# Kernel tuning notes

Measured on AMD Instinct MI355X. Metric: run time of the kernel, lower is better.

The kernel has to match this reference:

```python
import jax, jax.numpy as jnp
import numpy as np


def setup_inputs() -> dict:
    key = jax.random.key(0)
    ks = jax.random.split(key, 6)
    B, N, d = 8, 2048, 64
    h = jax.random.normal(ks[0], (B, N, d), dtype=jnp.float32)
    adj = jax.random.randint(ks[1], (B, N, N), 0, 2, dtype=jnp.int32)
    h_root = jax.random.normal(ks[2], (B, N), dtype=jnp.float32)
    weight = jax.random.normal(ks[3], (d, d), dtype=jnp.float32) * (1.0 / np.sqrt(d))
    a1 = jax.random.normal(ks[4], (d, 1), dtype=jnp.float32) * (1.0 / np.sqrt(d))
    a2 = jax.random.normal(ks[5], (d, 1), dtype=jnp.float32) * (1.0 / np.sqrt(d))
    return {"h": h, "adj": adj, "h_root": h_root, "weight": weight, "a1": a1, "a2": a2}


def reference(h, adj, h_root, weight, a1, a2):
    h0 = h
    hw = jax.nn.relu(jnp.matmul(h, weight))          # (B,N,d)
    t1 = jnp.matmul(hw, a1)                          # (B,N,1)
    t2 = jnp.matmul(hw, a2)                          # (B,N,1)
    # e[b,i,j] = relu(t1[b,i] + t2[b,j])  (broadcast, same as repeat/view in torch)
    e = jax.nn.relu(t1 + jnp.swapaxes(t2, -1, -2))   # (B,N,N)
    # FAITHFUL to source bug: pos0 = -9e15 * zeros_like(adj) == 0, so
    # non-edges get logit 0 (not -inf) before softmax.
    e = jnp.where(adj > 0, e, jnp.zeros_like(e))
    attention = jax.nn.softmax(e, axis=-1)           # (B,N,N)
    embedding = jnp.matmul(attention, hw)            # (B,N,d)
    # assign = h_root[:,:,None] @ ones(B,1,d) -> h_root broadcast over d;
    # assign > 0  <=>  h_root > 0 since ones are positive.
    assign = h_root[:, :, None] * jnp.ones((1, 1, hw.shape[-1]), dtype=hw.dtype)
    embedding = jnp.where(assign > 0, embedding, h0)
    return embedding
```

## Files before the change

kernel.cpp:

```cpp
#include <hip/hip_runtime.h>
#include <hip/hip_bf16.h>

#define BATCH 8
#define NN    2048
#define DD    64
#define BN    (BATCH * NN)
#define MWORDS 68

typedef __attribute__((ext_vector_type(8))) short bf16x8;
typedef __attribute__((ext_vector_type(4))) float f32x4;

static __device__ __forceinline__ unsigned f2bf_pk(float lo, float hi) {
  unsigned ul = __float_as_uint(lo);
  unsigned uh = __float_as_uint(hi);
  ul = (ul + 0x7fffu + ((ul >> 16) & 1u)) >> 16;
  uh = (uh + 0x7fffu + ((uh >> 16) & 1u)) & 0xffff0000u;
  return ul | uh;
}

__global__ __launch_bounds__(256) void kpack(
    const int* __restrict__ adj, const float* __restrict__ h_root,
    unsigned* __restrict__ masks) {
  const int row  = blockIdx.x * 4 + (threadIdx.x >> 6);
  const int lane = threadIdx.x & 63;
  if (h_root[row] <= 0.f) return;
  const int* ap = adj + (size_t)row * NN + lane * 32;
  unsigned word = 0;
#pragma unroll
  for (int i = 0; i < 8; ++i) {
    int4 v = *reinterpret_cast<const int4*>(ap + i * 4);
    word |= (v.x > 0 ? 1u : 0u) << (i * 4 + 0);
    word |= (v.y > 0 ? 1u : 0u) << (i * 4 + 1);
    word |= (v.z > 0 ? 1u : 0u) << (i * 4 + 2);
    word |= (v.w > 0 ? 1u : 0u) << (i * 4 + 3);
  }
  masks[(size_t)row * 64 + lane] = word;
}

__global__ __launch_bounds__(256) void k1_hw_t1_t2(
    const float* __restrict__ h, const float* __restrict__ W,
    const float* __restrict__ a1, const float* __restrict__ a2,
    unsigned short* __restrict__ hwT, float* __restrict__ t1, float* __restrict__ t2) {
  __shared__ float ht[64 * 36];
  __shared__ float Ws[64 * 64];
  __shared__ unsigned short bt[64 * 40];

  const int t  = threadIdx.x;
  const int r0 = blockIdx.x * 32;

#pragma unroll
  for (int r = 0; r < 4; ++r) {
    int f = t + 256 * r;
    reinterpret_cast<float4*>(Ws)[f] = reinterpret_cast<const float4*>(W)[f];
  }
#pragma unroll
  for (int r = 0; r < 2; ++r) {
    int f = t + 256 * r;
    int i = f >> 4, j4 = f & 15;
    float4 v = reinterpret_cast<const float4*>(h + (size_t)(r0 + i) * DD)[j4];
    ht[(4 * j4 + 0) * 36 + i] = v.x;
    ht[(4 * j4 + 1) * 36 + i] = v.y;
    ht[(4 * j4 + 2) * 36 + i] = v.z;
    ht[(4 * j4 + 3) * 36 + i] = v.w;
  }
  __syncthreads();

  const int trow = t >> 4, kcol = t & 15;
  float4 acc0 = make_float4(0.f, 0.f, 0.f, 0.f);
  float4 acc1 = make_float4(0.f, 0.f, 0.f, 0.f);

#pragma unroll 8
  for (int j = 0; j < 64; ++j) {
    float2 hv = *reinterpret_cast<const float2*>(&ht[j * 36 + 2 * trow]);
    float4 wv = reinterpret_cast<const float4*>(Ws)[j * 16 + kcol];
    acc0.x = fmaf(hv.x, wv.x, acc0.x); acc0.y = fmaf(hv.x, wv.y, acc0.y);
    acc0.z = fmaf(hv.x, wv.z, acc0.z); acc0.w = fmaf(hv.x, wv.w, acc0.w);
    acc1.x = fmaf(hv.y, wv.x, acc1.x); acc1.y = fmaf(hv.y, wv.y, acc1.y);
    acc1.z = fmaf(hv.y, wv.z, acc1.z); acc1.w = fmaf(hv.y, wv.w, acc1.w);
  }

  acc0.x = fmaxf(acc0.x, 0.f); acc0.y = fmaxf(acc0.y, 0.f);
  acc0.z = fmaxf(acc0.z, 0.f); acc0.w = fmaxf(acc0.w, 0.f);
  acc1.x = fmaxf(acc1.x, 0.f); acc1.y = fmaxf(acc1.y, 0.f);
  acc1.z = fmaxf(acc1.z, 0.f); acc1.w = fmaxf(acc1.w, 0.f);

  float4 a1v = reinterpret_cast<const float4*>(a1)[kcol];
  float4 a2v = reinterpret_cast<const float4*>(a2)[kcol];
  float s1_0 = acc0.x * a1v.x + acc0.y * a1v.y + acc0.z * a1v.z + acc0.w * a1v.w;
  float s1_1 = acc1.x * a1v.x + acc1.y * a1v.y + acc1.z * a1v.z + acc1.w * a1v.w;
  float s2_0 = acc0.x * a2v.x + acc0.y * a2v.y + acc0.z * a2v.z + acc0.w * a2v.w;
  float s2_1 = acc1.x * a2v.x + acc1.y * a2v.y + acc1.z * a2v.z + acc1.w * a2v.w;
#pragma unroll
  for (int mm = 1; mm <= 8; mm <<= 1) {
    s1_0 += __shfl_xor(s1_0, mm, 64);
    s1_1 += __shfl_xor(s1_1, mm, 64);
    s2_0 += __shfl_xor(s2_0, mm, 64);
    s2_1 += __shfl_xor(s2_1, mm, 64);
  }
  {
    int row = r0 + 2 * trow;
    if (kcol == 0) {
      t1[row] = s1_0; t1[row + 1] = s1_1;
      t2[row] = s2_0; t2[row + 1] = s2_1;
    }
  }

  {
    const float* a0 = &acc0.x;
    const float* a1p = &acc1.x;
#pragma unroll
    for (int c = 0; c < 4; ++c) {
      int k = 4 * kcol + c;
      *reinterpret_cast<unsigned*>(&bt[k * 40 + 2 * trow]) = f2bf_pk(a0[c], a1p[c]);
    }
  }
  __syncthreads();
  {
    int k = t >> 2, jp = t & 3;
    int g = k >> 4, n = k & 15;
    int bb = r0 >> 11;
    int jb = r0 & (NN - 1);
    int ks = jb >> 5;
    size_t base = ((((size_t)bb * (NN / 32) + ks) * 4 + g) * 64 + (jp * 16 + n)) * 8;
    *reinterpret_cast<int4*>(hwT + base) = *reinterpret_cast<const int4*>(&bt[k * 40 + jp * 8]);
  }
}

__global__ __launch_bounds__(256, 4) void k2_attn(
    const unsigned short* __restrict__ hwT, const unsigned* __restrict__ masks,
    const float* __restrict__ t1, const float* __restrict__ t2,
    const float* __restrict__ h, const float* __restrict__ h_root,
    float* __restrict__ out) {
  __shared__ unsigned maskS[16 * MWORDS];
  __shared__ float t2s[NN];
  __shared__ float os[4][16][68];
  __shared__ float denos[4][16];

  const int t    = threadIdx.x;
  const int b    = blockIdx.x >> 7;
  const int i0   = (blockIdx.x & 127) * 16;
  const int w    = t >> 6;
  const int lane = t & 63;
  const int m    = lane & 15;
  const int quad = lane >> 4;
  const int rowbase = b * NN + i0;

#pragma unroll
  for (int r = 0; r < 2; ++r)
    reinterpret_cast<float4*>(t2s)[t + 256 * r] =
        reinterpret_cast<const float4*>(t2 + b * NN)[t + 256 * r];

  {
    int row = t >> 4, w4 = t & 15;
    int4 mv = *reinterpret_cast<const int4*>(
        masks + ((size_t)(rowbase + row)) * 64 + w4 * 4);
    *reinterpret_cast<int4*>(&maskS[row * MWORDS + w4 * 4]) = mv;
  }
  __syncthreads();

  const float t1v = t1[rowbase + m];
  const int ks0 = w * 16;

  f32x4 acc[4];
#pragma unroll
  for (int g = 0; g < 4; ++g) acc[g] = (f32x4){0.f, 0.f, 0.f, 0.f};
  float den = 0.f;

  unsigned mcur = maskS[m * MWORDS + ks0];

#pragma unroll 1
  for (int kk = 0; kk < 16; ++kk) {
    const int ks = ks0 + kk;
    unsigned mnext = 0;
    if (kk + 1 < 16) mnext = maskS[m * MWORDS + ks + 1];

    const unsigned short* bp =
        hwT + ((((size_t)b * (NN / 32) + ks) * 4) * 64 + lane) * 8;
    bf16x8 B0 = *reinterpret_cast<const bf16x8*>(bp);
    bf16x8 B1 = *reinterpret_cast<const bf16x8*>(bp + 512);
    bf16x8 B2 = *reinterpret_cast<const bf16x8*>(bp + 1024);
    bf16x8 B3 = *reinterpret_cast<const bf16x8*>(bp + 1536);

    const float* t2p = &t2s[ks * 32 + quad * 8];
    float4 e0 = *reinterpret_cast<const float4*>(t2p);
    float4 e1 = *reinterpret_cast<const float4*>(t2p + 4);

    const unsigned mm8 = mcur >> (quad * 8);
    float p0 = (mm8 & 1u)   ? __expf(fmaxf(t1v + e0.x, 0.f)) : 1.f;
    float p1 = (mm8 & 2u)   ? __expf(fmaxf(t1v + e0.y, 0.f)) : 1.f;
    float p2 = (mm8 & 4u)   ? __expf(fmaxf(t1v + e0.z, 0.f)) : 1.f;
    float p3 = (mm8 & 8u)   ? __expf(fmaxf(t1v + e0.w, 0.f)) : 1.f;
    float p4 = (mm8 & 16u)  ? __expf(fmaxf(t1v + e1.x, 0.f)) : 1.f;
    float p5 = (mm8 & 32u)  ? __expf(fmaxf(t1v + e1.y, 0.f)) : 1.f;
    float p6 = (mm8 & 64u)  ? __expf(fmaxf(t1v + e1.z, 0.f)) : 1.f;
    float p7 = (mm8 & 128u) ? __expf(fmaxf(t1v + e1.w, 0.f)) : 1.f;
    den += ((p0 + p1) + (p2 + p3)) + ((p4 + p5) + (p6 + p7));

    union { bf16x8 v; unsigned u[4]; } Af;
    Af.u[0] = f2bf_pk(p0, p1); Af.u[1] = f2bf_pk(p2, p3);
    Af.u[2] = f2bf_pk(p4, p5); Af.u[3] = f2bf_pk(p6, p7);

    acc[0] = __builtin_amdgcn_mfma_f32_16x16x32_bf16(Af.v, B0, acc[0], 0, 0, 0);
    acc[1] = __builtin_amdgcn_mfma_f32_16x16x32_bf16(Af.v, B1, acc[1], 0, 0, 0);
    acc[2] = __builtin_amdgcn_mfma_f32_16x16x32_bf16(Af.v, B2, acc[2], 0, 0, 0);
    acc[3] = __builtin_amdgcn_mfma_f32_16x16x32_bf16(Af.v, B3, acc[3], 0, 0, 0);

    mcur = mnext;
  }

  den += __shfl_xor(den, 16, 64);
  den += __shfl_xor(den, 32, 64);
  if (quad == 0) denos[w][m] = den;

#pragma unroll
  for (int g = 0; g < 4; ++g)
#pragma unroll
    for (int r = 0; r < 4; ++r)
      os[w][quad * 4 + r][g * 16 + m] = acc[g][r];
  __syncthreads();

  {
    const int i = t >> 4, k4 = t & 15;
    float4 a = make_float4(0.f, 0.f, 0.f, 0.f);
    float d = 0.f;
#pragma unroll
    for (int ww = 0; ww < 4; ++ww) {
      float4 p = *reinterpret_cast<const float4*>(&os[ww][i][k4 * 4]);
      a.x += p.x; a.y += p.y; a.z += p.z; a.w += p.w;
      d += denos[ww][i];
    }
    const size_t row = (size_t)rowbase + i;
    float4 res;
    if (h_root[row] > 0.f) {
      const float inv = 1.f / d;
      res.x = a.x * inv; res.y = a.y * inv; res.z = a.z * inv; res.w = a.w * inv;
    } else {
      res = reinterpret_cast<const float4*>(h + row * DD)[k4];
    }
    reinterpret_cast<float4*>(out + row * DD)[k4] = res;
  }
}

extern "C" void kernel_launch(void* const* d_in, const int* in_sizes, int n_in,
                              void* d_out, int out_size, void* d_ws, size_t ws_size,
                              hipStream_t stream) {
  const float* h      = (const float*)d_in[0];
  const int*   adj    = (const int*)d_in[1];
  const float* h_root = (const float*)d_in[2];
  const float* W      = (const float*)d_in[3];
  const float* a1     = (const float*)d_in[4];
  const float* a2     = (const float*)d_in[5];
  float* out = (float*)d_out;

  unsigned short* hwT = (unsigned short*)d_ws;
  float* t1 = (float*)(hwT + (size_t)BN * DD);
  float* t2 = t1 + BN;
  unsigned* masks = (unsigned*)(t2 + BN);

  kpack<<<BN / 4, 256, 0, stream>>>(adj, h_root, masks);
  k1_hw_t1_t2<<<BN / 32, 256, 0, stream>>>(h, W, a1, a2, hwT, t1, t2);
  k2_attn<<<BATCH * (NN / 16), 256, 0, stream>>>(hwT, masks, t1, t2, h, h_root, out);
}
```

Before: 214.9 us.

## Merge mask packing into hw kernel and split attention into P-gen and GEMM

Mask packing and the hw/t1/t2 projection now run as one launch, with extra blocks doing the adjacency bit-packing, which saves a launch and lets both jobs share the GPU. The attention kernel is split in two. The first kernel computes the exp weights and row denominators and stores P as bf16 MFMA fragments in a global buffer. The second streams P and hwT through MFMA and normalises the result. The aim is to separate exp-heavy work from matrix-core work, at the cost of writing and re-reading a full B×N×N bf16 matrix through global memory.

```diff
diff --git a/kernel.cpp b/kernel.cpp
--- a/kernel.cpp
+++ b/kernel.cpp
@@ -18,29 +18,30 @@
   return ul | uh;
 }
 
-__global__ __launch_bounds__(256) void kpack(
-    const int* __restrict__ adj, const float* __restrict__ h_root,
-    unsigned* __restrict__ masks) {
-  const int row  = blockIdx.x * 4 + (threadIdx.x >> 6);
-  const int lane = threadIdx.x & 63;
-  if (h_root[row] <= 0.f) return;
-  const int* ap = adj + (size_t)row * NN + lane * 32;
-  unsigned word = 0;
-#pragma unroll
-  for (int i = 0; i < 8; ++i) {
-    int4 v = *reinterpret_cast<const int4*>(ap + i * 4);
-    word |= (v.x > 0 ? 1u : 0u) << (i * 4 + 0);
-    word |= (v.y > 0 ? 1u : 0u) << (i * 4 + 1);
-    word |= (v.z > 0 ? 1u : 0u) << (i * 4 + 2);
-    word |= (v.w > 0 ? 1u : 0u) << (i * 4 + 3);
-  }
-  masks[(size_t)row * 64 + lane] = word;
-}
-
-__global__ __launch_bounds__(256) void k1_hw_t1_t2(
+__global__ __launch_bounds__(256) void kA(
     const float* __restrict__ h, const float* __restrict__ W,
     const float* __restrict__ a1, const float* __restrict__ a2,
-    unsigned short* __restrict__ hwT, float* __restrict__ t1, float* __restrict__ t2) {
+    const int* __restrict__ adj, const float* __restrict__ h_root,
+    unsigned short* __restrict__ hwT, float* __restrict__ t1,
+    float* __restrict__ t2, unsigned* __restrict__ masks) {
+  if (blockIdx.x >= 512) {
+    const int row  = (blockIdx.x - 512) * 4 + (threadIdx.x >> 6);
+    const int lane = threadIdx.x & 63;
+    if (h_root[row] <= 0.f) return;
+    const int* ap = adj + (size_t)row * NN + lane * 32;
+    unsigned word = 0;
+#pragma unroll
+    for (int i = 0; i < 8; ++i) {
+      int4 v = *reinterpret_cast<const int4*>(ap + i * 4);
+      word |= (v.x > 0 ? 1u : 0u) << (i * 4 + 0);
+      word |= (v.y > 0 ? 1u : 0u) << (i * 4 + 1);
+      word |= (v.z > 0 ? 1u : 0u) << (i * 4 + 2);
+      word |= (v.w > 0 ? 1u : 0u) << (i * 4 + 3);
+    }
+    masks[(size_t)row * 64 + lane] = word;
+    return;
+  }
+
   __shared__ float ht[64 * 36];
   __shared__ float Ws[64 * 64];
   __shared__ unsigned short bt[64 * 40];
@@ -126,19 +127,19 @@
   }
 }
 
-__global__ __launch_bounds__(256, 4) void k2_attn(
-    const unsigned short* __restrict__ hwT, const unsigned* __restrict__ masks,
-    const float* __restrict__ t1, const float* __restrict__ t2,
-    const float* __restrict__ h, const float* __restrict__ h_root,
-    float* __restrict__ out) {
+__global__ __launch_bounds__(256, 4) void k2a_pgen(
+    const unsigned* __restrict__ masks, const float* __restrict__ t1,
+    const float* __restrict__ t2,
+    unsigned short* __restrict__ pfrag, float* __restrict__ den) {
   __shared__ unsigned maskS[16 * MWORDS];
   __shared__ float t2s[NN];
-  __shared__ float os[4][16][68];
-  __shared__ float denos[4][16];
+  __shared__ float t1s[16];
+  __shared__ float denP[4][16];
 
   const int t    = threadIdx.x;
-  const int b    = blockIdx.x >> 7;
-  const int i0   = (blockIdx.x & 127) * 16;
+  const int bid  = blockIdx.x;
+  const int b    = bid >> 7;
+  const int i0   = (bid & 127) * 16;
   const int w    = t >> 6;
   const int lane = t & 63;
   const int m    = lane & 15;
@@ -149,43 +150,29 @@
   for (int r = 0; r < 2; ++r)
     reinterpret_cast<float4*>(t2s)[t + 256 * r] =
         reinterpret_cast<const float4*>(t2 + b * NN)[t + 256 * r];
-
   {
     int row = t >> 4, w4 = t & 15;
     int4 mv = *reinterpret_cast<const int4*>(
-        masks + ((size_t)(rowbase + row)) * 64 + w4 * 4);
+        masks + (size_t)(rowbase + row) * 64 + w4 * 4);
     *reinterpret_cast<int4*>(&maskS[row * MWORDS + w4 * 4]) = mv;
   }
-  __syncthreads();
-
-  const float t1v = t1[rowbase + m];
+  if (t < 16) t1s[t] = t1[rowbase + t];
+  __syncthreads();
+
+  const float t1v = t1s[m];
   const int ks0 = w * 16;
-
-  f32x4 acc[4];
-#pragma unroll
-  for (int g = 0; g < 4; ++g) acc[g] = (f32x4){0.f, 0.f, 0.f, 0.f};
-  float den = 0.f;
-
-  unsigned mcur = maskS[m * MWORDS + ks0];
+  float den_acc = 0.f;
+  unsigned short* pout = pfrag + (((size_t)bid * 64 + ks0) * 64 + lane) * 8;
 
 #pragma unroll 1
   for (int kk = 0; kk < 16; ++kk) {
     const int ks = ks0 + kk;
-    unsigned mnext = 0;
-    if (kk + 1 < 16) mnext = maskS[m * MWORDS + ks + 1];
-
-    const unsigned short* bp =
-        hwT + ((((size_t)b * (NN / 32) + ks) * 4) * 64 + lane) * 8;
-    bf16x8 B0 = *reinterpret_cast<const bf16x8*>(bp);
-    bf16x8 B1 = *reinterpret_cast<const bf16x8*>(bp + 512);
-    bf16x8 B2 = *reinterpret_cast<const bf16x8*>(bp + 1024);
-    bf16x8 B3 = *reinterpret_cast<const bf16x8*>(bp + 1536);
-
+    const unsigned mw  = maskS[m * MWORDS + ks];
+    const unsigned mm8 = mw >> (quad * 8);
     const float* t2p = &t2s[ks * 32 + quad * 8];
     float4 e0 = *reinterpret_cast<const float4*>(t2p);
     float4 e1 = *reinterpret_cast<const float4*>(t2p + 4);
 
-    const unsigned mm8 = mcur >> (quad * 8);
     float p0 = (mm8 & 1u)   ? __expf(fmaxf(t1v + e0.x, 0.f)) : 1.f;
     float p1 = (mm8 & 2u)   ? __expf(fmaxf(t1v + e0.y, 0.f)) : 1.f;
     float p2 = (mm8 & 4u)   ? __expf(fmaxf(t1v + e0.z, 0.f)) : 1.f;
@@ -194,23 +181,63 @@
     float p5 = (mm8 & 32u)  ? __expf(fmaxf(t1v + e1.y, 0.f)) : 1.f;
     float p6 = (mm8 & 64u)  ? __expf(fmaxf(t1v + e1.z, 0.f)) : 1.f;
     float p7 = (mm8 & 128u) ? __expf(fmaxf(t1v + e1.w, 0.f)) : 1.f;
-    den += ((p0 + p1) + (p2 + p3)) + ((p4 + p5) + (p6 + p7));
-
-    union { bf16x8 v; unsigned u[4]; } Af;
-    Af.u[0] = f2bf_pk(p0, p1); Af.u[1] = f2bf_pk(p2, p3);
-    Af.u[2] = f2bf_pk(p4, p5); Af.u[3] = f2bf_pk(p6, p7);
-
-    acc[0] = __builtin_amdgcn_mfma_f32_16x16x32_bf16(Af.v, B0, acc[0], 0, 0, 0);
-    acc[1] = __builtin_amdgcn_mfma_f32_16x16x32_bf16(Af.v, B1, acc[1], 0, 0, 0);
-    acc[2] = __builtin_amdgcn_mfma_f32_16x16x32_bf16(Af.v, B2, acc[2], 0, 0, 0);
-    acc[3] = __builtin_amdgcn_mfma_f32_16x16x32_bf16(Af.v, B3, acc[3], 0, 0, 0);
-
-    mcur = mnext;
-  }
-
-  den += __shfl_xor(den, 16, 64);
-  den += __shfl_xor(den, 32, 64);
-  if (quad == 0) denos[w][m] = den;
+    den_acc += ((p0 + p1) + (p2 + p3)) + ((p4 + p5) + (p6 + p7));
+
+    int4 Af;
+    Af.x = (int)f2bf_pk(p0, p1);
+    Af.y = (int)f2bf_pk(p2, p3);
+    Af.z = (int)f2bf_pk(p4, p5);
+    Af.w = (int)f2bf_pk(p6, p7);
+    *reinterpret_cast<int4*>(pout + (size_t)kk * 512) = Af;
+  }
+
+  den_acc += __shfl_xor(den_acc, 16, 64);
+  den_acc += __shfl_xor(den_acc, 32, 64);
+  if (quad == 0) denP[w][m] = den_acc;
+  __syncthreads();
+  if (t < 16)
+    den[rowbase + t] = (denP[0][t] + denP[1][t]) + (denP[2][t] + denP[3][t]);
+}
+
+__global__ __launch_bounds__(256, 4) void k2b_gemm(
+    const unsigned short* __restrict__ hwT, const unsigned short* __restrict__ pfrag,
+    const float* __restrict__ den, const float* __restrict__ h,
+    const float* __restrict__ h_root, float* __restrict__ out) {
+  __shared__ float os[4][16][68];
+
+  const int t    = threadIdx.x;
+  const int bid  = blockIdx.x;
+  const int b    = bid >> 7;
+  const int i0   = (bid & 127) * 16;
+  const int w    = t >> 6;
+  const int lane = t & 63;
+  const int m    = lane & 15;
+  const int quad = lane >> 4;
+  const int rowbase = b * NN + i0;
+
+  f32x4 acc[4];
+#pragma unroll
+  for (int g = 0; g < 4; ++g) acc[g] = (f32x4){0.f, 0.f, 0.f, 0.f};
+
+  const int ks0 = w * 16;
+  const unsigned short* pin = pfrag + (((size_t)bid * 64 + ks0) * 64 + lane) * 8;
+  const unsigned short* bbase =
+      hwT + ((((size_t)b * (NN / 32) + ks0) * 4) * 64 + lane) * 8;
+
+#pragma unroll 1
+  for (int kk = 0; kk < 16; ++kk) {
+    bf16x8 A = *reinterpret_cast<const bf16x8*>(pin + (size_t)kk * 512);
+    const unsigned short* bp = bbase + (size_t)kk * 2048;
+    bf16x8 B0 = *reinterpret_cast<const bf16x8*>(bp);
+    bf16x8 B1 = *reinterpret_cast<const bf16x8*>(bp + 512);
+    bf16x8 B2 = *reinterpret_cast<const bf16x8*>(bp + 1024);
+    bf16x8 B3 = *reinterpret_cast<const bf16x8*>(bp + 1536);
+
+    acc[0] = __builtin_amdgcn_mfma_f32_16x16x32_bf16(A, B0, acc[0], 0, 0, 0);
+    acc[1] = __builtin_amdgcn_mfma_f32_16x16x32_bf16(A, B1, acc[1], 0, 0, 0);
+    acc[2] = __builtin_amdgcn_mfma_f32_16x16x32_bf16(A, B2, acc[2], 0, 0, 0);
+    acc[3] = __builtin_amdgcn_mfma_f32_16x16x32_bf16(A, B3, acc[3], 0, 0, 0);
+  }
 
 #pragma unroll
   for (int g = 0; g < 4; ++g)
@@ -222,17 +249,15 @@
   {
     const int i = t >> 4, k4 = t & 15;
     float4 a = make_float4(0.f, 0.f, 0.f, 0.f);
-    float d = 0.f;
 #pragma unroll
     for (int ww = 0; ww < 4; ++ww) {
       float4 p = *reinterpret_cast<const float4*>(&os[ww][i][k4 * 4]);
       a.x += p.x; a.y += p.y; a.z += p.z; a.w += p.w;
-      d += denos[ww][i];
     }
     const size_t row = (size_t)rowbase + i;
     float4 res;
     if (h_root[row] > 0.f) {
-      const float inv = 1.f / d;
+      const float inv = 1.f / den[row];
       res.x = a.x * inv; res.y = a.y * inv; res.z = a.z * inv; res.w = a.w * inv;
     } else {
       res = reinterpret_cast<const float4*>(h + row * DD)[k4];
@@ -255,9 +280,11 @@
   unsigned short* hwT = (unsigned short*)d_ws;
   float* t1 = (float*)(hwT + (size_t)BN * DD);
   float* t2 = t1 + BN;
-  unsigned* masks = (unsigned*)(t2 + BN);
-
-  kpack<<<BN / 4, 256, 0, stream>>>(adj, h_root, masks);
-  k1_hw_t1_t2<<<BN / 32, 256, 0, stream>>>(h, W, a1, a2, hwT, t1, t2);
-  k2_attn<<<BATCH * (NN / 16), 256, 0, stream>>>(hwT, masks, t1, t2, h, h_root, out);
-}
+  float* den = t2 + BN;
+  unsigned* masks = (unsigned*)(den + BN);
+  unsigned short* pfrag = (unsigned short*)(masks + (size_t)BN * 64);
+
+  kA<<<512 + BN / 4, 256, 0, stream>>>(h, W, a1, a2, adj, h_root, hwT, t1, t2, masks);
+  k2a_pgen<<<BATCH * 128, 256, 0, stream>>>(masks, t1, t2, pfrag, den);
+  k2b_gemm<<<BATCH * 128, 256, 0, stream>>>(hwT, pfrag, den, h, h_root, out);
+}
```

Result: slower. 221.0 us (+2.8%).
